# Kernel tuning notes

Measured on AMD Instinct MI355X. Metric: run time of the kernel, lower is better.

## Reference

```python
import jax, jax.numpy as jnp
import numpy as np

FLOAT_EPS = float(np.finfo(np.float32).eps)  # matches torch.finfo(torch.float32).eps


def setup_inputs() -> dict:
    key = jax.random.key(0)
    k0, k1, k2, k3, k4 = jax.random.split(key, 5)
    B, P, I, O, L = 16, 8192, 256, 128, 256  # batch, points, in_shapes, out_shapes, RNN_LATENT_SIZE
    x = jax.random.uniform(k0, (B, P, I), dtype=jnp.float32)
    latent_vector = jax.random.normal(k1, (B, L), dtype=jnp.float32)
    comp1 = 0.1 * jax.random.normal(k2, (L, I, O), dtype=jnp.float32)  # nn.init.normal_(std=0.1)
    comp2 = 0.1 * jax.random.normal(k3, (L, I, O), dtype=jnp.float32)
    temperature = jnp.full((1,), 2.0, dtype=jnp.float32)  # init.constant_(2)
    u = jax.random.uniform(k4, (B, 2, 1, I, O), dtype=jnp.float32)  # gumbel base noise (rand_like)
    return {"x": x, "latent_vector": latent_vector, "comp1": comp1,
            "comp2": comp2, "temperature": temperature, "u": u}


def reference(x, latent_vector, comp1, comp2, temperature, u):
    # mask_l/r: [B, I, O], softmax over the in-shapes axis (dim=-2)
    mask_l = jax.nn.softmax(jnp.einsum('bl,lio->bio', latent_vector, comp1), axis=-2)
    mask_r = jax.nn.softmax(jnp.einsum('bl,lio->bio', latent_vector, comp2), axis=-2)
    mask = jnp.stack([mask_l, mask_r], axis=1)[:, :, None]  # [B, 2, 1, I, O]

    # gumbel-softmax sampling: temperature clamp(eps, 2) then clamp_min(0.001)
    temp = jnp.maximum(jnp.clip(temperature, FLOAT_EPS, 2.0), 0.001)  # shape (1,)
    g = -jnp.log(-jnp.log(jnp.maximum(u, FLOAT_EPS)))
    mask_s = jax.nn.softmax((jnp.log(mask + FLOAT_EPS) + g) / temp, axis=-2)  # [B,2,1,I,O]

    # select: per-head broadcast-multiply-reduce == batched GEMM [B,P,I] x [B,2,I,O]
    sel = jnp.einsum('bpi,bkio->bpko', x, mask_s[:, :, 0])  # [B, P, 2, O]
    a, b = sel[:, :, 0], sel[:, :, 1]

    # arithmetic combine (union, intersection-ish, diffs) + clamp
    out = jnp.concatenate([a + b, a + b - 1.0, a - b, b - a], axis=-1)  # [B, P, 4*O]
    return jnp.clip(out, 0.0, 1.0)
```

## Files before the change

kernel.cpp:

```cpp
#include <hip/hip_runtime.h>
#include <hip/hip_bf16.h>

#define FLOAT_EPS 1.1920928955078125e-07f

typedef float f32x4 __attribute__((ext_vector_type(4)));
typedef short s16x8 __attribute__((ext_vector_type(8)));

#define B_ 16
#define P_ 8192
#define I_ 256
#define O_ 128
#define L_ 256
#define IO_ (I_*O_)

__device__ __forceinline__ float clip01(float v) {
    return fminf(fmaxf(v, 0.0f), 1.0f);
}

__global__ void rl_k0_lat(const float* __restrict__ lat, float* __restrict__ latT) {
    for (int e = threadIdx.x; e < B_ * L_; e += blockDim.x) {
        int b = e >> 8, l = e & 255;
        latT[l * 16 + b] = lat[e];
    }
}

__global__ __launch_bounds__(256) void rl_k1_logits(
        const float* __restrict__ latT,
        const float* __restrict__ c1, const float* __restrict__ c2,
        float* __restrict__ lgP) {
    const int n  = blockIdx.x * 256 + threadIdx.x;
    const int ks = blockIdx.y;
    const int lh = blockIdx.z;
    const float* __restrict__ C  = (ks ? c2 : c1) + (size_t)lh * 128 * IO_;
    const float* __restrict__ LT = latT + lh * 128 * 16;

    float acc[16];
#pragma unroll
    for (int b = 0; b < 16; ++b) acc[b] = 0.0f;

#pragma unroll 8
    for (int l = 0; l < 128; ++l) {
        float cv = C[(size_t)l * IO_ + n];
        const float4* lt = (const float4*)(LT + l * 16);
        float4 t0 = lt[0], t1 = lt[1], t2 = lt[2], t3 = lt[3];
        acc[0]  += t0.x * cv; acc[1]  += t0.y * cv; acc[2]  += t0.z * cv; acc[3]  += t0.w * cv;
        acc[4]  += t1.x * cv; acc[5]  += t1.y * cv; acc[6]  += t1.z * cv; acc[7]  += t1.w * cv;
        acc[8]  += t2.x * cv; acc[9]  += t2.y * cv; acc[10] += t2.z * cv; acc[11] += t2.w * cv;
        acc[12] += t3.x * cv; acc[13] += t3.y * cv; acc[14] += t3.z * cv; acc[15] += t3.w * cv;
    }
    float* o = lgP + ((size_t)(lh * 32 + ks * 16)) * IO_ + n;
#pragma unroll
    for (int b = 0; b < 16; ++b) o[(size_t)b * IO_] = acc[b];
}

__global__ __launch_bounds__(256) void rl_k2_mask(
        const float* __restrict__ lgP, const float* __restrict__ u,
        const float* __restrict__ temp_p, __hip_bfloat16* __restrict__ MT) {
    const int oo = threadIdx.x & 15;
    const int g  = threadIdx.x >> 4;
    const int o0 = blockIdx.x * 16;
    const int ks = blockIdx.y;
    const int b  = blockIdx.z;

    __shared__ float slab[I_][16];
    __shared__ float red[16][16];

    const float* __restrict__ z0 = lgP + (size_t)(ks * 16 + b) * IO_ + o0 + oo;
    const float* __restrict__ z1 = z0 + (size_t)32 * IO_;
    const float* __restrict__ up = u + ((size_t)b * 2 + ks) * IO_ + o0 + oo;

    float T = temp_p[0];
    T = fminf(fmaxf(T, FLOAT_EPS), 2.0f);
    T = fmaxf(T, 0.001f);
    const float rT = 1.0f / T;

    const int i0 = g * 16, i1 = i0 + 16;

    for (int i = i0; i < i1; ++i)
        slab[i][oo] = z0[(size_t)i * O_] + z1[(size_t)i * O_];
    __syncthreads();

    float m = -INFINITY;
    for (int i = i0; i < i1; ++i) m = fmaxf(m, slab[i][oo]);
    red[g][oo] = m; __syncthreads();
    m = -INFINITY;
#pragma unroll
    for (int j = 0; j < 16; ++j) m = fmaxf(m, red[j][oo]);
    __syncthreads();

    float S = 0.0f;
    for (int i = i0; i < i1; ++i) S += expf(slab[i][oo] - m);
    red[g][oo] = S; __syncthreads();
    S = 0.0f;
#pragma unroll
    for (int j = 0; j < 16; ++j) S += red[j][oo];
    __syncthreads();
    const float invS = 1.0f / S;

    float m2 = -INFINITY;
    for (int i = i0; i < i1; ++i) {
        float p  = expf(slab[i][oo] - m) * invS;
        float uu = fmaxf(up[(size_t)i * O_], FLOAT_EPS);
        float gg = -logf(-logf(uu));
        float s  = (logf(p + FLOAT_EPS) + gg) * rT;
        slab[i][oo] = s;
        m2 = fmaxf(m2, s);
    }
    red[g][oo] = m2; __syncthreads();
    m2 = -INFINITY;
#pragma unroll
    for (int j = 0; j < 16; ++j) m2 = fmaxf(m2, red[j][oo]);
    __syncthreads();

    float S2 = 0.0f;
    for (int i = i0; i < i1; ++i) S2 += expf(slab[i][oo] - m2);
    red[g][oo] = S2; __syncthreads();
    S2 = 0.0f;
#pragma unroll
    for (int j = 0; j < 16; ++j) S2 += red[j][oo];
    const float invS2 = 1.0f / S2;

    __hip_bfloat16* __restrict__ row = MT + ((size_t)(b * 256 + ks * 128 + o0 + oo)) * I_;
    for (int i = i0; i < i1; i += 2) {
        float v0 = expf(slab[i][oo]     - m2) * invS2;
        float v1 = expf(slab[i + 1][oo] - m2) * invS2;
        __hip_bfloat162 pk = __float22bfloat162_rn(make_float2(v0, v1));
        *(__hip_bfloat162*)(row + i) = pk;
    }
}

__global__ __launch_bounds__(512, 2) void rl_k3_gemm(
        const float* __restrict__ X, const __hip_bfloat16* __restrict__ MT,
        float* __restrict__ OUT) {
    const int tid  = threadIdx.x;
    const int lane = tid & 63, wid = tid >> 6;
    const int b    = blockIdx.y;

    __shared__ short Blds[256 * 256];

    const float* __restrict__ Xb           = X   + (size_t)b * P_ * I_;
    const __hip_bfloat16* __restrict__ MTb = MT  + (size_t)b * 65536;
    float* __restrict__ Ob                 = OUT + (size_t)b * P_ * 512;

#pragma unroll
    for (int it = 0; it < 16; ++it) {
        int idx = it * 512 + tid;
        int n = idx >> 5, c = idx & 31;
        s16x8 v = *(const s16x8*)(MTb + n * 256 + c * 8);
        *(s16x8*)((char*)Blds + n * 512 + ((c * 16) ^ ((n & 7) << 4))) = v;
    }
    __syncthreads();

    const int l15 = lane & 15, lhi = lane >> 4;

    for (int itm = 0; itm < 2; ++itm) {
        const int rowb = blockIdx.x * 512 + itm * 256 + wid * 32 + l15;
        const float* __restrict__ A0 = Xb + (size_t)rowb * I_ + lhi * 8;

        s16x8 af[2][8];
#pragma unroll
        for (int fm = 0; fm < 2; ++fm)
#pragma unroll
        for (int kk = 0; kk < 8; ++kk) {
            const float* src = A0 + fm * 16 * I_ + kk * 32;
            float4 f0 = *(const float4*)src;
            float4 f1 = *(const float4*)(src + 4);
            union { s16x8 v; __hip_bfloat162 h[4]; } cv;
            cv.h[0] = __float22bfloat162_rn(make_float2(f0.x, f0.y));
            cv.h[1] = __float22bfloat162_rn(make_float2(f0.z, f0.w));
            cv.h[2] = __float22bfloat162_rn(make_float2(f1.x, f1.y));
            cv.h[3] = __float22bfloat162_rn(make_float2(f1.z, f1.w));
            af[fm][kk] = cv.v;
        }

        f32x4 acc[2][16];
#pragma unroll
        for (int i = 0; i < 2; ++i)
#pragma unroll
        for (int j = 0; j < 16; ++j) acc[i][j] = (f32x4){0.f, 0.f, 0.f, 0.f};

#pragma unroll
        for (int kk = 0; kk < 8; ++kk) {
            const int kb = kk * 64 + lhi * 16;
#pragma unroll
            for (int fn = 0; fn < 16; ++fn) {
                int n = fn * 16 + l15;
                s16x8 bf = *(const s16x8*)((const char*)Blds + n * 512 + (kb ^ ((n & 7) << 4)));
                acc[0][fn] = __builtin_amdgcn_mfma_f32_16x16x32_bf16(af[0][kk], bf, acc[0][fn], 0, 0, 0);
                acc[1][fn] = __builtin_amdgcn_mfma_f32_16x16x32_bf16(af[1][kk], bf, acc[1][fn], 0, 0, 0);
            }
        }

        const int cb = l15, rb = lhi * 4;
#pragma unroll
        for (int fm = 0; fm < 2; ++fm)
#pragma unroll
        for (int fn = 0; fn < 8; ++fn)
#pragma unroll
        for (int r = 0; r < 4; ++r) {
            int p = blockIdx.x * 512 + itm * 256 + wid * 32 + fm * 16 + rb + r;
            float a  = acc[fm][fn][r];
            float bb = acc[fm][fn + 8][r];
            float* op = Ob + (size_t)p * 512 + fn * 16 + cb;
            op[0]   = clip01(a + bb);
            op[128] = clip01(a + bb - 1.0f);
            op[256] = clip01(a - bb);
            op[384] = clip01(bb - a);
        }
    }
}

extern "C" void kernel_launch(void* const* d_in, const int* in_sizes, int n_in,
                              void* d_out, int out_size, void* d_ws, size_t ws_size,
                              hipStream_t stream) {
    const float* x    = (const float*)d_in[0];
    const float* lat  = (const float*)d_in[1];
    const float* c1   = (const float*)d_in[2];
    const float* c2   = (const float*)d_in[3];
    const float* temp = (const float*)d_in[4];
    const float* u    = (const float*)d_in[5];
    float* out = (float*)d_out;

    char* ws = (char*)d_ws;
    float*          lgP  = (float*)ws;
    __hip_bfloat16* MT   = (__hip_bfloat16*)(ws + (8 << 20));
    float*          latT = (float*)(ws + (10 << 20));

    rl_k0_lat   <<<1, 256, 0, stream>>>(lat, latT);
    rl_k1_logits<<<dim3(128, 2, 2), 256, 0, stream>>>(latT, c1, c2, lgP);
    rl_k2_mask  <<<dim3(8, 2, 16), 256, 0, stream>>>(lgP, u, temp, MT);
    rl_k3_gemm  <<<dim3(16, 16), 512, 0, stream>>>(x, MT, out);
}
```

Before: 147.9 us.

## Prefetch next X row chunk in GEMM and drop latent transpose kernel

The GEMM kernel now handles 64 rows per wave in four 16-row chunks. Raw fp32 X for the next chunk is loaded into registers while the current chunk runs its MFMAs, which overlaps global load latency with compute and cuts accumulator registers. A separate launch for the latent transpose is removed; the logits kernel now reads the latent vector directly with scalar-broadcast loads. This saves one launch but gives up the float4 loads of the transposed layout.

```diff
diff --git a/kernel.cpp b/kernel.cpp
--- a/kernel.cpp
+++ b/kernel.cpp
@@ -17,36 +17,26 @@
     return fminf(fmaxf(v, 0.0f), 1.0f);
 }
 
-__global__ void rl_k0_lat(const float* __restrict__ lat, float* __restrict__ latT) {
-    for (int e = threadIdx.x; e < B_ * L_; e += blockDim.x) {
-        int b = e >> 8, l = e & 255;
-        latT[l * 16 + b] = lat[e];
-    }
-}
-
 __global__ __launch_bounds__(256) void rl_k1_logits(
-        const float* __restrict__ latT,
+        const float* __restrict__ lat,
         const float* __restrict__ c1, const float* __restrict__ c2,
         float* __restrict__ lgP) {
     const int n  = blockIdx.x * 256 + threadIdx.x;
     const int ks = blockIdx.y;
     const int lh = blockIdx.z;
     const float* __restrict__ C  = (ks ? c2 : c1) + (size_t)lh * 128 * IO_;
-    const float* __restrict__ LT = latT + lh * 128 * 16;
+    const int lbase = lh * 128;
 
     float acc[16];
 #pragma unroll
     for (int b = 0; b < 16; ++b) acc[b] = 0.0f;
 
-#pragma unroll 8
+#pragma unroll 4
     for (int l = 0; l < 128; ++l) {
         float cv = C[(size_t)l * IO_ + n];
-        const float4* lt = (const float4*)(LT + l * 16);
-        float4 t0 = lt[0], t1 = lt[1], t2 = lt[2], t3 = lt[3];
-        acc[0]  += t0.x * cv; acc[1]  += t0.y * cv; acc[2]  += t0.z * cv; acc[3]  += t0.w * cv;
-        acc[4]  += t1.x * cv; acc[5]  += t1.y * cv; acc[6]  += t1.z * cv; acc[7]  += t1.w * cv;
-        acc[8]  += t2.x * cv; acc[9]  += t2.y * cv; acc[10] += t2.z * cv; acc[11] += t2.w * cv;
-        acc[12] += t3.x * cv; acc[13] += t3.y * cv; acc[14] += t3.z * cv; acc[15] += t3.w * cv;
+#pragma unroll
+        for (int b = 0; b < 16; ++b)
+            acc[b] += lat[b * L_ + lbase + l] * cv;
     }
     float* o = lgP + ((size_t)(lh * 32 + ks * 16)) * IO_ + n;
 #pragma unroll
@@ -152,32 +142,43 @@
     __syncthreads();
 
     const int l15 = lane & 15, lhi = lane >> 4;
-
-    for (int itm = 0; itm < 2; ++itm) {
-        const int rowb = blockIdx.x * 512 + itm * 256 + wid * 32 + l15;
-        const float* __restrict__ A0 = Xb + (size_t)rowb * I_ + lhi * 8;
-
-        s16x8 af[2][8];
-#pragma unroll
-        for (int fm = 0; fm < 2; ++fm)
+    const int rowbase = blockIdx.x * 512 + wid * 64 + l15;
+    const int rb = lhi * 4;
+
+    float4 raw[16];
+    {
+        const float* s0 = Xb + (size_t)rowbase * I_ + lhi * 8;
 #pragma unroll
         for (int kk = 0; kk < 8; ++kk) {
-            const float* src = A0 + fm * 16 * I_ + kk * 32;
-            float4 f0 = *(const float4*)src;
-            float4 f1 = *(const float4*)(src + 4);
+            raw[2 * kk]     = *(const float4*)(s0 + kk * 32);
+            raw[2 * kk + 1] = *(const float4*)(s0 + kk * 32 + 4);
+        }
+    }
+
+    for (int c = 0; c < 4; ++c) {
+        s16x8 af[8];
+#pragma unroll
+        for (int kk = 0; kk < 8; ++kk) {
+            float4 f0 = raw[2 * kk], f1 = raw[2 * kk + 1];
             union { s16x8 v; __hip_bfloat162 h[4]; } cv;
             cv.h[0] = __float22bfloat162_rn(make_float2(f0.x, f0.y));
             cv.h[1] = __float22bfloat162_rn(make_float2(f0.z, f0.w));
             cv.h[2] = __float22bfloat162_rn(make_float2(f1.x, f1.y));
             cv.h[3] = __float22bfloat162_rn(make_float2(f1.z, f1.w));
-            af[fm][kk] = cv.v;
-        }
-
-        f32x4 acc[2][16];
-#pragma unroll
-        for (int i = 0; i < 2; ++i)
-#pragma unroll
-        for (int j = 0; j < 16; ++j) acc[i][j] = (f32x4){0.f, 0.f, 0.f, 0.f};
+            af[kk] = cv.v;
+        }
+        if (c < 3) {
+            const float* s1 = Xb + (size_t)(rowbase + (c + 1) * 16) * I_ + lhi * 8;
+#pragma unroll
+            for (int kk = 0; kk < 8; ++kk) {
+                raw[2 * kk]     = *(const float4*)(s1 + kk * 32);
+                raw[2 * kk + 1] = *(const float4*)(s1 + kk * 32 + 4);
+            }
+        }
+
+        f32x4 acc[16];
+#pragma unroll
+        for (int j = 0; j < 16; ++j) acc[j] = (f32x4){0.f, 0.f, 0.f, 0.f};
 
 #pragma unroll
         for (int kk = 0; kk < 8; ++kk) {
@@ -186,22 +187,18 @@
             for (int fn = 0; fn < 16; ++fn) {
                 int n = fn * 16 + l15;
                 s16x8 bf = *(const s16x8*)((const char*)Blds + n * 512 + (kb ^ ((n & 7) << 4)));
-                acc[0][fn] = __builtin_amdgcn_mfma_f32_16x16x32_bf16(af[0][kk], bf, acc[0][fn], 0, 0, 0);
-                acc[1][fn] = __builtin_amdgcn_mfma_f32_16x16x32_bf16(af[1][kk], bf, acc[1][fn], 0, 0, 0);
+                acc[fn] = __builtin_amdgcn_mfma_f32_16x16x32_bf16(af[kk], bf, acc[fn], 0, 0, 0);
             }
         }
 
-        const int cb = l15, rb = lhi * 4;
-#pragma unroll
-        for (int fm = 0; fm < 2; ++fm)
+        const int prow = blockIdx.x * 512 + wid * 64 + c * 16 + rb;
 #pragma unroll
         for (int fn = 0; fn < 8; ++fn)
 #pragma unroll
         for (int r = 0; r < 4; ++r) {
-            int p = blockIdx.x * 512 + itm * 256 + wid * 32 + fm * 16 + rb + r;
-            float a  = acc[fm][fn][r];
-            float bb = acc[fm][fn + 8][r];
-            float* op = Ob + (size_t)p * 512 + fn * 16 + cb;
+            float a  = acc[fn][r];
+            float bb = acc[fn + 8][r];
+            float* op = Ob + (size_t)(prow + r) * 512 + fn * 16 + l15;
             op[0]   = clip01(a + bb);
             op[128] = clip01(a + bb - 1.0f);
             op[256] = clip01(a - bb);
@@ -222,12 +219,10 @@
     float* out = (float*)d_out;
 
     char* ws = (char*)d_ws;
-    float*          lgP  = (float*)ws;
-    __hip_bfloat16* MT   = (__hip_bfloat16*)(ws + (8 << 20));
-    float*          latT = (float*)(ws + (10 << 20));
-
-    rl_k0_lat   <<<1, 256, 0, stream>>>(lat, latT);
-    rl_k1_logits<<<dim3(128, 2, 2), 256, 0, stream>>>(latT, c1, c2, lgP);
+    float*          lgP = (float*)ws;
+    __hip_bfloat16* MT  = (__hip_bfloat16*)(ws + (8 << 20));
+
+    rl_k1_logits<<<dim3(128, 2, 2), 256, 0, stream>>>(lat, c1, c2, lgP);
     rl_k2_mask  <<<dim3(8, 2, 16), 256, 0, stream>>>(lgP, u, temp, MT);
     rl_k3_gemm  <<<dim3(16, 16), 512, 0, stream>>>(x, MT, out);
 }
```

New measurement: 149.5 us. Within noise of the previous version (+1.1%).
